# Kernel tuning notes

Hardware: AMD Instinct MI355X
Metric: run time of the kernel (lower is better)

The kernel has to match this reference:

```python
import jax, jax.numpy as jnp
import numpy as np

N_NODES = 50000

def setup_inputs() -> dict:
    key = jax.random.key(0)
    k1, k2, k3, k4, k5 = jax.random.split(key, 5)
    feat = jax.random.normal(k1, (N_NODES, 192), dtype=jnp.float32)
    edge_feat = jax.random.normal(k2, (800000, 64), dtype=jnp.float32)
    src = jax.random.randint(k3, (800000,), 0, N_NODES, dtype=jnp.int32)
    dst = jax.random.randint(k4, (800000,), 0, N_NODES, dtype=jnp.int32)
    weight = jax.random.normal(k5, (256, 256), dtype=jnp.float32) * (1.0 / np.sqrt(256.0))
    bias = jnp.zeros((256,), dtype=jnp.float32)
    return {"feat": feat, "edge_feat": edge_feat, "src": src, "dst": dst,
            "weight": weight, "bias": bias}


def reference(feat, edge_feat, src, dst, weight, bias):
    N = feat.shape[0]
    ones_e = jnp.ones(src.shape[0], dtype=jnp.float32)
    # out-degree normalization of source features (pre-aggregation)
    out_deg = jnp.clip(jax.ops.segment_sum(ones_e, src, num_segments=N), 1.0, None)
    feat_n = feat * (out_deg ** -0.5)[:, None]            # [N, d_node]
    # message = concat(src_feat_norm, edge_feat); sum over dst.
    # segment_sum distributes over concat, so aggregate parts separately
    # (avoids materializing the [E, d_node+d_edge] message tensor).
    h_src = jax.ops.segment_sum(feat_n[src], dst, num_segments=N)   # [N, d_node]
    h_edge = jax.ops.segment_sum(edge_feat, dst, num_segments=N)    # [N, d_edge]
    h = jnp.concatenate([h_src, h_edge], axis=1)          # [N, in_feats]
    rst = h @ weight                                      # [N, out_feats]
    # in-degree normalization (post-aggregation)
    in_deg = jnp.clip(jax.ops.segment_sum(ones_e, dst, num_segments=N), 1.0, None)
    rst = rst * (in_deg ** -0.5)[:, None] + bias
    return rst
```

## Files before the change

kernel.cpp:

```cpp
#include <hip/hip_runtime.h>

#define NN 50000
#define NE 800000
#define DIN 256
#define DOUT 256

typedef __attribute__((ext_vector_type(8))) short bf16x8;
typedef __attribute__((ext_vector_type(4))) float f32x4;

__device__ __forceinline__ unsigned short f2bf(float x) {
    unsigned int u = __builtin_bit_cast(unsigned int, x);
    u += 0x7fffu + ((u >> 16) & 1u);
    return (unsigned short)(u >> 16);
}
__device__ __forceinline__ float bf2f(unsigned short b) {
    return __builtin_bit_cast(float, ((unsigned int)b) << 16);
}


__global__ __launch_bounds__(256) void zero_meta(int* __restrict__ p, int n) {
    int i = blockIdx.x * 256 + threadIdx.x;
    if (i < n) p[i] = 0;
}

__global__ __launch_bounds__(256) void count_kernel(const int* __restrict__ src,
                                                    const int* __restrict__ dst,
                                                    int* __restrict__ in_cnt,
                                                    int* __restrict__ out_cnt) {
    int e = blockIdx.x * 256 + threadIdx.x;
    if (e < NE) {
        atomicAdd(in_cnt + dst[e], 1);
        atomicAdd(out_cnt + src[e], 1);
    }
}

__global__ __launch_bounds__(256) void scan1(const int* __restrict__ cnt,
                                             int* __restrict__ row_off,
                                             int* __restrict__ bsum) {
    __shared__ int tmp[256];
    int tid = threadIdx.x;
    int i = blockIdx.x * 256 + tid;
    int v = (i < NN) ? cnt[i] : 0;
    tmp[tid] = v;
    __syncthreads();
#pragma unroll
    for (int off = 1; off < 256; off <<= 1) {
        int t = (tid >= off) ? tmp[tid - off] : 0;
        __syncthreads();
        if (tid >= off) tmp[tid] += t;
        __syncthreads();
    }
    if (i < NN) row_off[i] = tmp[tid] - v;
    if (tid == 255) bsum[blockIdx.x] = tmp[255];
}

__global__ __launch_bounds__(256) void scan2(int* __restrict__ bsum, int nb) {
    __shared__ int tmp[256];
    int tid = threadIdx.x;
    int v = (tid < nb) ? bsum[tid] : 0;
    tmp[tid] = v;
    __syncthreads();
#pragma unroll
    for (int off = 1; off < 256; off <<= 1) {
        int t = (tid >= off) ? tmp[tid - off] : 0;
        __syncthreads();
        if (tid >= off) tmp[tid] += t;
        __syncthreads();
    }
    if (tid < nb) bsum[tid] = tmp[tid] - v;
}

__global__ __launch_bounds__(256) void scan3(int* __restrict__ row_off,
                                             int* __restrict__ cursor,
                                             float* __restrict__ odeg_inv,
                                             const int* __restrict__ out_cnt,
                                             const int* __restrict__ bsum) {
    int i = blockIdx.x * 256 + threadIdx.x;
    if (i < NN) {
        int v = row_off[i] + bsum[i >> 8];
        row_off[i] = v;
        cursor[i] = v;
        odeg_inv[i] = rsqrtf((float)max(out_cnt[i], 1));
    }
    if (i == NN) row_off[NN] = NE;
}

__global__ __launch_bounds__(256) void wconv(const float* __restrict__ W,
                                             unsigned short* __restrict__ wt) {
    int n = blockIdx.x, k = threadIdx.x;
    wt[n * 256 + k] = f2bf(W[k * 256 + n]);
}

__global__ __launch_bounds__(256) void featconv(const float* __restrict__ feat,
                                                const float* __restrict__ odeg_inv,
                                                unsigned short* __restrict__ featn) {
    int node = blockIdx.x * 4 + (threadIdx.x >> 6);
    int lane = threadIdx.x & 63;
    if (node >= NN || lane >= 48) return;
    float s = odeg_inv[node];
    float4 v = *(const float4*)(feat + (size_t)node * 192 + lane * 4);
    ushort4 o;
    o.x = f2bf(v.x * s); o.y = f2bf(v.y * s);
    o.z = f2bf(v.z * s); o.w = f2bf(v.w * s);
    *(ushort4*)(featn + (size_t)node * 192 + lane * 4) = o;
}

__global__ __launch_bounds__(256) void fill_kernel(const int* __restrict__ src,
                                                   const int* __restrict__ dst,
                                                   int* __restrict__ cursor,
                                                   int2* __restrict__ perm2) {
    int e = blockIdx.x * 256 + threadIdx.x;
    if (e < NE) {
        int d = dst[e];
        int pos = atomicAdd(cursor + d, 1);
        perm2[pos] = make_int2(e, src[e]);
    }
}

__global__ __launch_bounds__(256) void aggregate_kernel(const unsigned short* __restrict__ featn,
                                                        const float* __restrict__ edge_feat,
                                                        const int* __restrict__ row_off,
                                                        const int2* __restrict__ perm2,
                                                        unsigned short* __restrict__ h_bf) {
    int node = blockIdx.x * 4 + (threadIdx.x >> 6);
    int lane = threadIdx.x & 63;
    if (node >= NN) return;
    int start = row_off[node];
    int end   = row_off[node + 1];

    float4 acc = make_float4(0.f, 0.f, 0.f, 0.f);

    if (lane < 48) {
        const unsigned short* fb = featn + lane * 4;
        for (int i = start; i < end; i += 8) {
            int2 p[8];
#pragma unroll
            for (int j = 0; j < 8; ++j) p[j] = perm2[min(i + j, end - 1)];
            ushort4 u[8];
#pragma unroll
            for (int j = 0; j < 8; ++j)
                u[j] = *(const ushort4*)(fb + (size_t)p[j].y * 192);
#pragma unroll
            for (int j = 0; j < 8; ++j) {
                float w = (i + j < end) ? 1.f : 0.f;
                acc.x = fmaf(bf2f(u[j].x), w, acc.x);
                acc.y = fmaf(bf2f(u[j].y), w, acc.y);
                acc.z = fmaf(bf2f(u[j].z), w, acc.z);
                acc.w = fmaf(bf2f(u[j].w), w, acc.w);
            }
        }
    } else {
        const float* eb = edge_feat + (lane - 48) * 4;
        for (int i = start; i < end; i += 8) {
            int2 p[8];
#pragma unroll
            for (int j = 0; j < 8; ++j) p[j] = perm2[min(i + j, end - 1)];
            float4 v[8];
#pragma unroll
            for (int j = 0; j < 8; ++j)
                v[j] = *(const float4*)(eb + (size_t)p[j].x * 64);
#pragma unroll
            for (int j = 0; j < 8; ++j) {
                float w = (i + j < end) ? 1.f : 0.f;
                acc.x = fmaf(v[j].x, w, acc.x);
                acc.y = fmaf(v[j].y, w, acc.y);
                acc.z = fmaf(v[j].z, w, acc.z);
                acc.w = fmaf(v[j].w, w, acc.w);
            }
        }
    }

    ushort4 o;
    o.x = f2bf(acc.x); o.y = f2bf(acc.y);
    o.z = f2bf(acc.z); o.w = f2bf(acc.w);
    *(ushort4*)(h_bf + (size_t)node * 256 + lane * 4) = o;
}

__global__ __launch_bounds__(256) void gemm_mfma(const unsigned short* __restrict__ h_bf,
                                                 const unsigned short* __restrict__ wt_bf,
                                                 const float* __restrict__ bias,
                                                 const int* __restrict__ row_off,
                                                 float* __restrict__ out) {
    int wave = threadIdx.x >> 6;
    int lane = threadIdx.x & 63;
    int m16  = lane & 15;
    int quad = lane >> 4;
    int rbase = blockIdx.x * 16;
    int cbase = wave * 64;

    const unsigned short* arow = h_bf + (size_t)(rbase + m16) * 256 + quad * 8;
    const unsigned short* b0p = wt_bf + (size_t)(cbase +  0 + m16) * 256 + quad * 8;
    const unsigned short* b1p = wt_bf + (size_t)(cbase + 16 + m16) * 256 + quad * 8;
    const unsigned short* b2p = wt_bf + (size_t)(cbase + 32 + m16) * 256 + quad * 8;
    const unsigned short* b3p = wt_bf + (size_t)(cbase + 48 + m16) * 256 + quad * 8;

    f32x4 acc0 = {0.f, 0.f, 0.f, 0.f};
    f32x4 acc1 = {0.f, 0.f, 0.f, 0.f};
    f32x4 acc2 = {0.f, 0.f, 0.f, 0.f};
    f32x4 acc3 = {0.f, 0.f, 0.f, 0.f};

#pragma unroll
    for (int k0 = 0; k0 < 256; k0 += 32) {
        bf16x8 a  = *(const bf16x8*)(arow + k0);
        bf16x8 b0 = *(const bf16x8*)(b0p + k0);
        bf16x8 b1 = *(const bf16x8*)(b1p + k0);
        bf16x8 b2 = *(const bf16x8*)(b2p + k0);
        bf16x8 b3 = *(const bf16x8*)(b3p + k0);
        acc0 = __builtin_amdgcn_mfma_f32_16x16x32_bf16(a, b0, acc0, 0, 0, 0);
        acc1 = __builtin_amdgcn_mfma_f32_16x16x32_bf16(a, b1, acc1, 0, 0, 0);
        acc2 = __builtin_amdgcn_mfma_f32_16x16x32_bf16(a, b2, acc2, 0, 0, 0);
        acc3 = __builtin_amdgcn_mfma_f32_16x16x32_bf16(a, b3, acc3, 0, 0, 0);
    }

    int grow0 = rbase + quad * 4;
    float s[4];
    int ro_prev = row_off[grow0];
#pragma unroll
    for (int r = 0; r < 4; ++r) {
        int nx = row_off[grow0 + r + 1];
        s[r] = rsqrtf((float)max(nx - ro_prev, 1));
        ro_prev = nx;
    }

    float bv0 = bias[cbase +  0 + m16];
    float bv1 = bias[cbase + 16 + m16];
    float bv2 = bias[cbase + 32 + m16];
    float bv3 = bias[cbase + 48 + m16];

#pragma unroll
    for (int r = 0; r < 4; ++r) {
        size_t rowoff = (size_t)(grow0 + r) * DOUT;
        out[rowoff + cbase +  0 + m16] = acc0[r] * s[r] + bv0;
        out[rowoff + cbase + 16 + m16] = acc1[r] * s[r] + bv1;
        out[rowoff + cbase + 32 + m16] = acc2[r] * s[r] + bv2;
        out[rowoff + cbase + 48 + m16] = acc3[r] * s[r] + bv3;
    }
}

extern "C" void kernel_launch(void* const* d_in, const int* in_sizes, int n_in,
                              void* d_out, int out_size, void* d_ws, size_t ws_size,
                              hipStream_t stream) {
    const float* feat      = (const float*)d_in[0];
    const float* edge_feat = (const float*)d_in[1];
    const int*   src       = (const int*)d_in[2];
    const int*   dst       = (const int*)d_in[3];
    const float* W         = (const float*)d_in[4];
    const float* bias      = (const float*)d_in[5];
    float* out = (float*)d_out;

    unsigned short* h_bf    = (unsigned short*)d_ws;
    unsigned short* wt_bf   = h_bf + (size_t)NN * DIN;
    unsigned short* featn   = wt_bf + 256 * 256;
    int*   row_off  = (int*)(featn + (size_t)NN * 192);
    float* odeg_inv = (float*)(row_off + NN + 2);
    int*   cursor   = (int*)(odeg_inv + NN);
    int*   bsum     = cursor + NN;
    int2*  perm2    = (int2*)(bsum + 256);
    int*   in_cnt   = (int*)perm2;
    int*   out_cnt  = in_cnt + NN;

    const int SCAN_BLOCKS = (NN + 255) / 256;

    zero_meta<<<(2 * NN + 255) / 256, 256, 0, stream>>>(in_cnt, 2 * NN);
    count_kernel<<<(NE + 255) / 256, 256, 0, stream>>>(src, dst, in_cnt, out_cnt);
    scan1<<<SCAN_BLOCKS, 256, 0, stream>>>(in_cnt, row_off, bsum);
    scan2<<<1, 256, 0, stream>>>(bsum, SCAN_BLOCKS);
    scan3<<<(NN + 256) / 256, 256, 0, stream>>>(row_off, cursor, odeg_inv, out_cnt, bsum);
    wconv<<<256, 256, 0, stream>>>(W, wt_bf);
    featconv<<<(NN + 3) / 4, 256, 0, stream>>>(feat, odeg_inv, featn);
    fill_kernel<<<(NE + 255) / 256, 256, 0, stream>>>(src, dst, cursor, perm2);
    aggregate_kernel<<<(NN + 3) / 4, 256, 0, stream>>>(featn, edge_feat, row_off,
                                                       perm2, h_bf);
    gemm_mfma<<<NN / 16, 256, 0, stream>>>(h_bf, wt_bf, bias, row_off, out);
}
```

Baseline: 585.4 us.

## Scatter edge features into dst-sorted bf16 buffer during fill

The fill kernel now reads each edge's 64 fp32 features sequentially, converts them to bf16, and writes them to their CSR slot. Aggregation then reads them contiguously per destination node instead of gathering fp32 rows through a permutation index. The src index array shrinks from int2 to int. The cost is an extra 800000x64 bf16 write pass and a larger workspace requirement, with a fallback to the old path when the workspace is too small.

```diff
diff --git a/kernel.cpp b/kernel.cpp
--- a/kernel.cpp
+++ b/kernel.cpp
@@ -7,6 +7,7 @@
 
 typedef __attribute__((ext_vector_type(8))) short bf16x8;
 typedef __attribute__((ext_vector_type(4))) float f32x4;
+typedef __attribute__((ext_vector_type(8))) unsigned short u16x8;
 
 __device__ __forceinline__ unsigned short f2bf(float x) {
     unsigned int u = __builtin_bit_cast(unsigned int, x);
@@ -108,7 +109,86 @@
 __global__ __launch_bounds__(256) void fill_kernel(const int* __restrict__ src,
                                                    const int* __restrict__ dst,
                                                    int* __restrict__ cursor,
-                                                   int2* __restrict__ perm2) {
+                                                   int* __restrict__ perm,
+                                                   unsigned short* __restrict__ eperm,
+                                                   const float* __restrict__ edge_feat) {
+    int e = blockIdx.x * 256 + threadIdx.x;
+    if (e >= NE) return;
+    int pos = atomicAdd(cursor + dst[e], 1);
+    perm[pos] = src[e];
+    const float* ef = edge_feat + (size_t)e * 64;
+    unsigned short* op = eperm + (size_t)pos * 64;
+#pragma unroll
+    for (int k = 0; k < 8; ++k) {
+        float4 a = *(const float4*)(ef + k * 8);
+        float4 b = *(const float4*)(ef + k * 8 + 4);
+        u16x8 o;
+        o[0] = f2bf(a.x); o[1] = f2bf(a.y); o[2] = f2bf(a.z); o[3] = f2bf(a.w);
+        o[4] = f2bf(b.x); o[5] = f2bf(b.y); o[6] = f2bf(b.z); o[7] = f2bf(b.w);
+        *(u16x8*)(op + k * 8) = o;
+    }
+}
+
+__global__ __launch_bounds__(256) void aggregate_kernel(const unsigned short* __restrict__ featn,
+                                                        const unsigned short* __restrict__ eperm,
+                                                        const int* __restrict__ row_off,
+                                                        const int* __restrict__ perm,
+                                                        unsigned short* __restrict__ h_bf) {
+    int node = blockIdx.x * 4 + (threadIdx.x >> 6);
+    int lane = threadIdx.x & 63;
+    if (node >= NN) return;
+    int start = row_off[node];
+    int end   = row_off[node + 1];
+
+    float4 acc = make_float4(0.f, 0.f, 0.f, 0.f);
+
+    if (lane < 48) {
+        const unsigned short* fb = featn + lane * 4;
+        for (int i = start; i < end; i += 8) {
+            int s[8];
+#pragma unroll
+            for (int j = 0; j < 8; ++j) s[j] = perm[min(i + j, end - 1)];
+            ushort4 u[8];
+#pragma unroll
+            for (int j = 0; j < 8; ++j)
+                u[j] = *(const ushort4*)(fb + (size_t)s[j] * 192);
+#pragma unroll
+            for (int j = 0; j < 8; ++j) {
+                float w = (i + j < end) ? 1.f : 0.f;
+                acc.x = fmaf(bf2f(u[j].x), w, acc.x);
+                acc.y = fmaf(bf2f(u[j].y), w, acc.y);
+                acc.z = fmaf(bf2f(u[j].z), w, acc.z);
+                acc.w = fmaf(bf2f(u[j].w), w, acc.w);
+            }
+        }
+    } else {
+        const unsigned short* eb = eperm + (lane - 48) * 4;
+        for (int i = start; i < end; i += 8) {
+            ushort4 u[8];
+#pragma unroll
+            for (int j = 0; j < 8; ++j)
+                u[j] = *(const ushort4*)(eb + (size_t)min(i + j, end - 1) * 64);
+#pragma unroll
+            for (int j = 0; j < 8; ++j) {
+                float w = (i + j < end) ? 1.f : 0.f;
+                acc.x = fmaf(bf2f(u[j].x), w, acc.x);
+                acc.y = fmaf(bf2f(u[j].y), w, acc.y);
+                acc.z = fmaf(bf2f(u[j].z), w, acc.z);
+                acc.w = fmaf(bf2f(u[j].w), w, acc.w);
+            }
+        }
+    }
+
+    ushort4 o;
+    o.x = f2bf(acc.x); o.y = f2bf(acc.y);
+    o.z = f2bf(acc.z); o.w = f2bf(acc.w);
+    *(ushort4*)(h_bf + (size_t)node * 256 + lane * 4) = o;
+}
+
+__global__ __launch_bounds__(256) void fill_fb(const int* __restrict__ src,
+                                               const int* __restrict__ dst,
+                                               int* __restrict__ cursor,
+                                               int2* __restrict__ perm2) {
     int e = blockIdx.x * 256 + threadIdx.x;
     if (e < NE) {
         int d = dst[e];
@@ -117,11 +197,11 @@
     }
 }
 
-__global__ __launch_bounds__(256) void aggregate_kernel(const unsigned short* __restrict__ featn,
-                                                        const float* __restrict__ edge_feat,
-                                                        const int* __restrict__ row_off,
-                                                        const int2* __restrict__ perm2,
-                                                        unsigned short* __restrict__ h_bf) {
+__global__ __launch_bounds__(256) void aggregate_fb(const unsigned short* __restrict__ featn,
+                                                    const float* __restrict__ edge_feat,
+                                                    const int* __restrict__ row_off,
+                                                    const int2* __restrict__ perm2,
+                                                    unsigned short* __restrict__ h_bf) {
     int node = blockIdx.x * 4 + (threadIdx.x >> 6);
     int lane = threadIdx.x & 63;
     if (node >= NN) return;
@@ -255,9 +335,14 @@
     float* odeg_inv = (float*)(row_off + NN + 2);
     int*   cursor   = (int*)(odeg_inv + NN);
     int*   bsum     = cursor + NN;
-    int2*  perm2    = (int2*)(bsum + 256);
-    int*   in_cnt   = (int*)perm2;
+    int*   perm     = bsum + 256;
+    unsigned short* eperm = (unsigned short*)(perm + NE);
+    int2*  perm2    = (int2*)perm;
+    int*   in_cnt   = perm;
     int*   out_cnt  = in_cnt + NN;
+
+    size_t need = (size_t)((char*)(eperm + (size_t)NE * 64) - (char*)d_ws);
+    bool big_ws = (ws_size >= need);
 
     const int SCAN_BLOCKS = (NN + 255) / 256;
 
@@ -268,8 +353,15 @@
     scan3<<<(NN + 256) / 256, 256, 0, stream>>>(row_off, cursor, odeg_inv, out_cnt, bsum);
     wconv<<<256, 256, 0, stream>>>(W, wt_bf);
     featconv<<<(NN + 3) / 4, 256, 0, stream>>>(feat, odeg_inv, featn);
-    fill_kernel<<<(NE + 255) / 256, 256, 0, stream>>>(src, dst, cursor, perm2);
-    aggregate_kernel<<<(NN + 3) / 4, 256, 0, stream>>>(featn, edge_feat, row_off,
+    if (big_ws) {
+        fill_kernel<<<(NE + 255) / 256, 256, 0, stream>>>(src, dst, cursor, perm,
+                                                          eperm, edge_feat);
+        aggregate_kernel<<<(NN + 3) / 4, 256, 0, stream>>>(featn, eperm, row_off,
+                                                           perm, h_bf);
+    } else {
+        fill_fb<<<(NE + 255) / 256, 256, 0, stream>>>(src, dst, cursor, perm2);
+        aggregate_fb<<<(NN + 3) / 4, 256, 0, stream>>>(featn, edge_feat, row_off,
                                                        perm2, h_bf);
+    }
     gemm_mfma<<<NN / 16, 256, 0, stream>>>(h_bf, wt_bf, bias, row_off, out);
 }
```

Measured after the change: 608.1 us. 3.9% more time.
